# Performance work log

Hardware: AMD Instinct MI355X
Metric: run time of the kernel (lower is better)

## Reference

```python
import jax, jax.numpy as jnp
import numpy as np

B, S, D = 2, 2048, 2048
H, HD = 16, 128
P = 2048  # past (cached) kv length


def setup_inputs() -> dict:
    key = jax.random.key(0)
    ks = jax.random.split(key, 12)
    sw = 1.0 / np.sqrt(D)
    inp = {
        "x": jax.random.normal(ks[0], (B, S, D), jnp.float32),
        "past_k": jax.random.normal(ks[1], (B, H, P, HD), jnp.float32),
        "past_v": jax.random.normal(ks[2], (B, H, P, HD), jnp.float32),
        "Wq": jax.random.normal(ks[3], (D, D), jnp.float32) * sw,
        "bq": jax.random.normal(ks[4], (D,), jnp.float32) * 0.01,
        "Wk": jax.random.normal(ks[5], (D, D), jnp.float32) * sw,
        "bk": jax.random.normal(ks[6], (D,), jnp.float32) * 0.01,
        "Wv": jax.random.normal(ks[7], (D, D), jnp.float32) * sw,
        "bv": jax.random.normal(ks[8], (D,), jnp.float32) * 0.01,
        "Wo": jax.random.normal(ks[9], (D, D), jnp.float32) * sw,
        "bo": jax.random.normal(ks[10], (D,), jnp.float32) * 0.01,
    }
    return inp


def _heads(t):
    # [B, S, D] -> [B, H, S, HD]
    return t.reshape(B, -1, H, HD).transpose(0, 2, 1, 3)


def reference(x, past_k, past_v, Wq, bq, Wk, bk, Wv, bv, Wo, bo):
    # QKV projections (separate weights, _qkv_same_embed_dim=False path)
    q = _heads(x @ Wq.T + bq)          # [B,H,S,HD]
    k_new = _heads(x @ Wk.T + bk)      # [B,H,S,HD]
    v_new = _heads(x @ Wv.T + bv)

    # KV cache append
    k_cached = jnp.concatenate([past_k, k_new], axis=2)  # [B,H,P+S,HD]
    v_cached = jnp.concatenate([past_v, v_new], axis=2)
    cached_len = P + S

    # Manual attention path (query_seq_len != cached_seq_len)
    scale = 1.0 / np.sqrt(HD)
    scores = jnp.einsum('bhqd,bhkd->bhqk', q, k_cached) * scale  # [B,H,S,P+S]
    q_pos = jnp.arange(cached_len - S, cached_len)[:, None]
    k_pos = jnp.arange(cached_len)[None, :]
    mask = q_pos >= k_pos  # offset causal mask [S, P+S]
    scores = jnp.where(mask, scores, -jnp.inf)
    attn = jax.nn.softmax(scores, axis=-1)
    out = jnp.einsum('bhqk,bhkd->bhqd', attn, v_cached)  # [B,H,S,HD]

    out = out.transpose(0, 2, 1, 3).reshape(B, S, D)
    return out @ Wo.T + bo
```

## Files before the change

kernel.cpp:

```cpp
#include <hip/hip_runtime.h>

typedef unsigned short u16;
typedef __attribute__((ext_vector_type(4))) float f32x4;
typedef __attribute__((ext_vector_type(16))) float f32x16;
typedef __attribute__((ext_vector_type(8))) short s16x8;
typedef __attribute__((ext_vector_type(2))) unsigned int u32x2v;

#define CEXP 0.12751742929f

static __device__ __forceinline__ u16 f2bf(float x) {
  unsigned u = __float_as_uint(x);
  u = u + 0x7fffu + ((u >> 16) & 1u);
  return (u16)(u >> 16);
}
static __device__ __forceinline__ unsigned cvtpk(float a, float b) {
  unsigned r;
  asm("v_cvt_pk_bf16_f32 %0, %1, %2" : "=v"(r) : "v"(a), "v"(b));
  return r;
}
static __device__ __forceinline__ u32x2v pswap(unsigned a, unsigned b) {
  return __builtin_amdgcn_permlane32_swap(a, b, false, false);
}
static __device__ __forceinline__ f32x4 fzero() { f32x4 z; z[0]=0.f; z[1]=0.f; z[2]=0.f; z[3]=0.f; return z; }
static __device__ __forceinline__ f32x4 mfma16(s16x8 a, s16x8 b, f32x4 c) {
  return __builtin_amdgcn_mfma_f32_16x16x32_bf16(a, b, c, 0, 0, 0);
}
static __device__ __forceinline__ f32x16 mfma32(s16x8 a, s16x8 b, f32x16 c) {
  return __builtin_amdgcn_mfma_f32_32x32x16_bf16(a, b, c, 0, 0, 0);
}
static __device__ __forceinline__ void gld16(const void* g, void* l) {
  __builtin_amdgcn_global_load_lds((const __attribute__((address_space(1))) void*)g,
                                   (__attribute__((address_space(3))) void*)l, 16, 0, 0);
}

__global__ void cvt_kernel(const float* __restrict__ s, u16* __restrict__ d, int n4, int lg) {
  int stride = gridDim.x * blockDim.x;
  for (int i4 = blockIdx.x * blockDim.x + threadIdx.x; i4 < n4; i4 += stride) {
    int i = i4 * 4;
    float4 v = *reinterpret_cast<const float4*>(s + i);
    size_t di = (size_t)i + ((size_t)(i >> lg) << lg);
    ushort4 o;
    o.x = f2bf(v.x); o.y = f2bf(v.y); o.z = f2bf(v.z); o.w = f2bf(v.w);
    *reinterpret_cast<ushort4*>(d + di) = o;
  }
}

__global__ void transpose_past_v(const float* __restrict__ src, u16* __restrict__ dst) {
  __shared__ u16 tile[64 * 138];
  int bh = blockIdx.y, pt = blockIdx.x;
  const float* s = src + ((size_t)bh * 2048 + (size_t)pt * 64) * 128;
  int t = threadIdx.x;
#pragma unroll
  for (int it = 0; it < 8; ++it) {
    int idx = it * 1024 + t * 4;
    int row = idx >> 7, col = idx & 127;
    float4 v = *reinterpret_cast<const float4*>(s + idx);
    u16* d = &tile[row * 138 + col];
    d[0] = f2bf(v.x); d[1] = f2bf(v.y); d[2] = f2bf(v.z); d[3] = f2bf(v.w);
  }
  __syncthreads();
  size_t dbase = (size_t)bh * 128 * 4096 + (size_t)pt * 64;
#pragma unroll
  for (int it = 0; it < 32; ++it) {
    int o = it * 256 + t;
    int dd = o >> 6, pos = o & 63;
    dst[dbase + (size_t)dd * 4096 + pos] = tile[pos * 138 + dd];
  }
}

__global__ void transpose_new_v(const u16* __restrict__ src, u16* __restrict__ dst) {
  __shared__ u16 tile[64 * 138];
  int bh = blockIdx.y, pt = blockIdx.x;
  const u16* s = src + ((size_t)bh * 2048 + (size_t)pt * 64) * 128;
  int t = threadIdx.x;
#pragma unroll
  for (int it = 0; it < 8; ++it) {
    int idx = it * 1024 + t * 4;
    int row = idx >> 7, col = idx & 127;
    ushort4 v = *reinterpret_cast<const ushort4*>(s + idx);
    u16* d = &tile[row * 138 + col];
    d[0] = v.x; d[1] = v.y; d[2] = v.z; d[3] = v.w;
  }
  __syncthreads();
  size_t dbase = (size_t)bh * 128 * 4096 + 2048 + (size_t)pt * 64;
#pragma unroll
  for (int it = 0; it < 32; ++it) {
    int o = it * 256 + t;
    int dd = o >> 6, pos = o & 63;
    dst[dbase + (size_t)dd * 4096 + pos] = tile[pos * 138 + dd];
  }
}

static __device__ __forceinline__ void gemm_core(const u16* __restrict__ A, const u16* __restrict__ Wn,
                                                 int m0, char* ldsb, f32x4 (&acc)[4][4]) {
  const int tid = threadIdx.x;
  const int w = tid >> 6, lane = tid & 63, g = lane >> 4, ln = lane & 15;
#pragma unroll
  for (int mi = 0; mi < 4; ++mi)
#pragma unroll
    for (int ni = 0; ni < 4; ++ni) acc[mi][ni] = fzero();

  auto stage = [&](int buf, int k0) {
#pragma unroll
    for (int i = 0; i < 2; ++i) {
      int c = w * 2 + i;
      int p = c * 1024 + lane * 16;
      int row = p >> 6;
      int colb = (p & 63) ^ ((row & 3) << 4);
      const u16* sa = A + (size_t)(m0 + row) * 2048 + k0 + (colb >> 1);
      const u16* sw = Wn + (size_t)row * 2048 + k0 + (colb >> 1);
      char* da = ldsb + buf * 16384 + c * 1024;
      gld16(sa, da);
      gld16(sw, da + 8192);
    }
  };
  stage(0, 0);
  const int wr = w >> 1, wc = w & 1;
  for (int kt = 0; kt < 64; ++kt) {
    int cur = kt & 1;
    if (kt < 63) {
      stage(cur ^ 1, (kt + 1) * 32);
      asm volatile("s_waitcnt vmcnt(4)\n\ts_barrier" ::: "memory");
    } else {
      asm volatile("s_waitcnt vmcnt(0)\n\ts_barrier" ::: "memory");
    }
    const char* bp = ldsb + cur * 16384;
    s16x8 af[4], bw[4];
#pragma unroll
    for (int mi = 0; mi < 4; ++mi) {
      int row = wr * 64 + mi * 16 + ln;
      int lin = row * 64 + g * 16;
      af[mi] = *reinterpret_cast<const s16x8*>(bp + (lin ^ ((row & 3) << 4)));
    }
#pragma unroll
    for (int ni = 0; ni < 4; ++ni) {
      int row = wc * 64 + ni * 16 + ln;
      int lin = row * 64 + g * 16;
      bw[ni] = *reinterpret_cast<const s16x8*>(bp + 8192 + (lin ^ ((row & 3) << 4)));
    }
#pragma unroll
    for (int mi = 0; mi < 4; ++mi)
#pragma unroll
      for (int ni = 0; ni < 4; ++ni)
        acc[mi][ni] = mfma16(af[mi], bw[ni], acc[mi][ni]);
    asm volatile("s_waitcnt lgkmcnt(0)\n\ts_barrier" ::: "memory");
  }
}

__global__ __launch_bounds__(256, 3) void qkv_gemm(const u16* __restrict__ xb,
    const u16* __restrict__ wq, const u16* __restrict__ wk, const u16* __restrict__ wv,
    const float* __restrict__ bq, const float* __restrict__ bk, const float* __restrict__ bv,
    u16* __restrict__ outq, u16* __restrict__ kc, u16* __restrict__ outv) {
  __shared__ char ldsb[32768];
  int m0 = blockIdx.x * 128;
  int ny = blockIdx.y;
  int wsel = ny >> 4, n0 = (ny & 15) * 128;
  const u16* W; const float* bias; u16* dst; int lrow, off;
  if (wsel == 0)      { W = wq; bias = bq; dst = outq; lrow = 2048; off = 0; }
  else if (wsel == 1) { W = wk; bias = bk; dst = kc;   lrow = 4096; off = 2048; }
  else                { W = wv; bias = bv; dst = outv; lrow = 2048; off = 0; }
  f32x4 acc[4][4];
  gemm_core(xb, W + (size_t)n0 * 2048, m0, ldsb, acc);
  const int tid = threadIdx.x, w = tid >> 6, lane = tid & 63, g = lane >> 4, ln = lane & 15;
  const int wr = w >> 1, wc = w & 1;
#pragma unroll
  for (int ni = 0; ni < 4; ++ni) {
    int j = n0 + wc * 64 + ni * 16 + ln;
    float bcol = bias[j];
    int h = j >> 7, hd = j & 127;
#pragma unroll
    for (int mi = 0; mi < 4; ++mi) {
#pragma unroll
      for (int r = 0; r < 4; ++r) {
        int rowg = m0 + wr * 64 + mi * 16 + g * 4 + r;
        int b = rowg >> 11, s = rowg & 2047;
        float val = acc[mi][ni][r] + bcol;
        dst[((size_t)(b * 16 + h) * lrow + off + s) * 128 + hd] = f2bf(val);
      }
    }
  }
}

__global__ __launch_bounds__(256, 3) void proj_gemm(const u16* __restrict__ ao, const u16* __restrict__ wo,
    const float* __restrict__ bo, float* __restrict__ out) {
  __shared__ char ldsb[32768];
  int m0 = blockIdx.x * 128, n0 = blockIdx.y * 128;
  f32x4 acc[4][4];
  gemm_core(ao, wo + (size_t)n0 * 2048, m0, ldsb, acc);
  const int tid = threadIdx.x, w = tid >> 6, lane = tid & 63, g = lane >> 4, ln = lane & 15;
  const int wr = w >> 1, wc = w & 1;
#pragma unroll
  for (int ni = 0; ni < 4; ++ni) {
    int j = n0 + wc * 64 + ni * 16 + ln;
    float bcol = bo[j];
#pragma unroll
    for (int mi = 0; mi < 4; ++mi) {
#pragma unroll
      for (int r = 0; r < 4; ++r) {
        int rowg = m0 + wr * 64 + mi * 16 + g * 4 + r;
        out[(size_t)rowg * 2048 + j] = acc[mi][ni][r] + bcol;
      }
    }
  }
}

__global__ __launch_bounds__(256, 2) void attn_kernel(const u16* __restrict__ Qb,
    const u16* __restrict__ Kc, const u16* __restrict__ Vt, u16* __restrict__ Ao) {
  __shared__ char lds[65536];
  const int tid = threadIdx.x, w = tid >> 6, lane = tid & 63;
  const int hi = lane >> 5, l5 = lane & 31;
  const int bh = blockIdx.x;
  const int qy = blockIdx.y;
  const int qbk = (qy & 8) ? (15 - (qy & 7)) : qy;
  const int b = bh >> 4, h = bh & 15;
  const u16* Qbh = Qb + (size_t)bh * 2048 * 128;
  const u16* Kbh = Kc + (size_t)bh * 4096 * 128;
  const u16* Vbh = Vt + (size_t)bh * 128 * 4096;

  const int qrow0 = qbk * 128 + w * 32;
  const int qp = 2048 + qrow0 + l5;
  const int qpmin = 2048 + qrow0;
  const int ntiles = (2048 + qbk * 128 + 128) >> 6;

  s16x8 qf[8];
#pragma unroll
  for (int kc = 0; kc < 8; ++kc)
    qf[kc] = *reinterpret_cast<const s16x8*>(Qbh + (size_t)(qrow0 + l5) * 128 + kc * 16 + hi * 8);

  f32x16 o[4];
#pragma unroll
  for (int dt = 0; dt < 4; ++dt)
#pragma unroll
    for (int i = 0; i < 16; ++i) o[dt][i] = 0.f;
  float mrun = -3e38f, lrun = 0.f;

  auto stage = [&](int buf, int kv0) {
    char* base = lds + buf * 32768;
#pragma unroll
    for (int i = 0; i < 4; ++i) {
      int p = (w * 4 + i) * 1024 + lane * 16;
      int row = p >> 8;
      int colb = (p & 255) ^ ((row & 7) << 4);
      gld16(Kbh + (size_t)(kv0 + row) * 128 + (colb >> 1), base + (w * 4 + i) * 1024);
      int vrow = p >> 7;
      int vcol = (p & 127) ^ ((vrow & 7) << 4);
      gld16(Vbh + (size_t)vrow * 4096 + kv0 + (vcol >> 1), base + 16384 + (w * 4 + i) * 1024);
    }
  };

  stage(0, 0);
  for (int t = 0; t < ntiles; ++t) {
    const int kv0 = t * 64;
    const int cur = t & 1;
    if (t + 1 < ntiles) {
      stage(cur ^ 1, kv0 + 64);
      asm volatile("s_waitcnt vmcnt(8)\n\ts_barrier" ::: "memory");
    } else {
      asm volatile("s_waitcnt vmcnt(0)\n\ts_barrier" ::: "memory");
    }
    const char* Kl = lds + cur * 32768;
    const char* Vl = Kl + 16384;
    if (kv0 <= qpmin + 31) {
      f32x16 s0, s1;
#pragma unroll
      for (int i = 0; i < 16; ++i) { s0[i] = 0.f; s1[i] = 0.f; }
      __builtin_amdgcn_s_setprio(1);
#pragma unroll
      for (int kc = 0; kc < 8; ++kc) {
        {
          int row = l5;
          int lin = row * 256 + kc * 32 + hi * 16;
          s16x8 a = *reinterpret_cast<const s16x8*>(Kl + (lin ^ ((row & 7) << 4)));
          s0 = mfma32(a, qf[kc], s0);
        }
        {
          int row = 32 + l5;
          int lin = row * 256 + kc * 32 + hi * 16;
          s16x8 a = *reinterpret_cast<const s16x8*>(Kl + (lin ^ ((row & 7) << 4)));
          s1 = mfma32(a, qf[kc], s1);
        }
      }
      __builtin_amdgcn_s_setprio(0);
      if (kv0 + 63 > qpmin) {
#pragma unroll
        for (int i = 0; i < 16; ++i) {
          int r0 = (i & 3) + 8 * (i >> 2) + 4 * hi;
          if (kv0 + r0 > qp) s0[i] = -3e38f;
          if (kv0 + 32 + r0 > qp) s1[i] = -3e38f;
        }
      }
      float pm = fmaxf(s0[0], s0[1]);
#pragma unroll
      for (int i = 2; i < 16; i += 2) pm = fmaxf(fmaxf(pm, s0[i]), s0[i + 1]);
#pragma unroll
      for (int i = 0; i < 16; i += 2) pm = fmaxf(fmaxf(pm, s1[i]), s1[i + 1]);
      {
        u32x2v rr = pswap(__float_as_uint(pm), __float_as_uint(pm));
        pm = fmaxf(pm, __uint_as_float(hi ? rr[0] : rr[1]));
      }
      float mnew = (pm > mrun + 8.f) ? pm : mrun;
      float fsc = exp2f((mrun - mnew) * CEXP);
      mrun = mnew;
      float r0 = 0.f, r1 = 0.f, r2 = 0.f, r3 = 0.f;
#pragma unroll
      for (int i = 0; i < 16; i += 4) {
        float p0 = exp2f((s0[i] - mnew) * CEXP);
        float p1 = exp2f((s0[i + 1] - mnew) * CEXP);
        float p2 = exp2f((s0[i + 2] - mnew) * CEXP);
        float p3 = exp2f((s0[i + 3] - mnew) * CEXP);
        s0[i] = p0; s0[i + 1] = p1; s0[i + 2] = p2; s0[i + 3] = p3;
        r0 += p0; r1 += p1; r2 += p2; r3 += p3;
      }
#pragma unroll
      for (int i = 0; i < 16; i += 4) {
        float p0 = exp2f((s1[i] - mnew) * CEXP);
        float p1 = exp2f((s1[i + 1] - mnew) * CEXP);
        float p2 = exp2f((s1[i + 2] - mnew) * CEXP);
        float p3 = exp2f((s1[i + 3] - mnew) * CEXP);
        s1[i] = p0; s1[i + 1] = p1; s1[i + 2] = p2; s1[i + 3] = p3;
        r0 += p0; r1 += p1; r2 += p2; r3 += p3;
      }
      float rs = (r0 + r1) + (r2 + r3);
      {
        u32x2v rr = pswap(__float_as_uint(rs), __float_as_uint(rs));
        rs += __uint_as_float(hi ? rr[0] : rr[1]);
      }
      lrun = lrun * fsc + rs;
      if (!__all(fsc == 1.f)) {
#pragma unroll
        for (int dt = 0; dt < 4; ++dt)
#pragma unroll
          for (int i = 0; i < 16; ++i) o[dt][i] *= fsc;
      }
      s16x8 pb[4];
#pragma unroll
      for (int c2 = 0; c2 < 4; ++c2) {
        const f32x16& sv = (c2 & 2) ? s1 : s0;
        const int b0 = (c2 & 1) * 8;
        unsigned x0 = cvtpk(sv[b0 + 0], sv[b0 + 1]);
        unsigned x1 = cvtpk(sv[b0 + 2], sv[b0 + 3]);
        unsigned y0 = cvtpk(sv[b0 + 4], sv[b0 + 5]);
        unsigned y1 = cvtpk(sv[b0 + 6], sv[b0 + 7]);
        u32x2v q0 = pswap(x0, y0);
        u32x2v q1 = pswap(x1, y1);
        union { unsigned u[4]; s16x8 v; } pu;
        pu.u[0] = q0[0]; pu.u[1] = q1[0]; pu.u[2] = q0[1]; pu.u[3] = q1[1];
        pb[c2] = pu.v;
      }
      __builtin_amdgcn_s_setprio(1);
#pragma unroll
      for (int dt = 0; dt < 4; ++dt) {
#pragma unroll
        for (int c2 = 0; c2 < 4; ++c2) {
          int row = dt * 32 + l5;
          int lin = row * 128 + c2 * 32 + hi * 16;
          s16x8 va = *reinterpret_cast<const s16x8*>(Vl + (lin ^ ((row & 7) << 4)));
          o[dt] = mfma32(va, pb[c2], o[dt]);
        }
      }
      __builtin_amdgcn_s_setprio(0);
    }
    asm volatile("s_waitcnt lgkmcnt(0)\n\ts_barrier" ::: "memory");
  }

  float li = 1.f / lrun;
#pragma unroll
  for (int dt = 0; dt < 4; ++dt)
#pragma unroll
    for (int i = 0; i < 16; ++i) o[dt][i] *= li;
  const int qb = w * 32 + l5;
#pragma unroll
  for (int dt = 0; dt < 4; ++dt) {
#pragma unroll
    for (int rg = 0; rg < 4; ++rg) {
      int d0 = dt * 32 + rg * 8 + hi * 4;
      unsigned w0 = cvtpk(o[dt][rg * 4 + 0], o[dt][rg * 4 + 1]);
      unsigned w1 = cvtpk(o[dt][rg * 4 + 2], o[dt][rg * 4 + 3]);
      int lin = qb * 256 + d0 * 2;
      int phys = lin ^ ((qb & 7) << 4);
      *reinterpret_cast<uint2*>(lds + phys) = make_uint2(w0, w1);
    }
  }
  __syncthreads();
  const int qr = tid >> 4, c16 = tid & 15;
#pragma unroll
  for (int it = 0; it < 8; ++it) {
    int q = qr + it * 16;
    int phys = (q * 256 + c16 * 16) ^ ((q & 7) << 4);
    s16x8 v = *reinterpret_cast<const s16x8*>(lds + phys);
    *reinterpret_cast<s16x8*>(Ao + ((size_t)(b * 2048 + qbk * 128 + q)) * 2048 + h * 128 + c16 * 8) = v;
  }
}

extern "C" void kernel_launch(void* const* d_in, const int* in_sizes, int n_in,
                              void* d_out, int out_size, void* d_ws, size_t ws_size,
                              hipStream_t stream) {
  const float* x      = (const float*)d_in[0];
  const float* past_k = (const float*)d_in[1];
  const float* past_v = (const float*)d_in[2];
  const float* Wq = (const float*)d_in[3];
  const float* bq = (const float*)d_in[4];
  const float* Wk = (const float*)d_in[5];
  const float* bk = (const float*)d_in[6];
  const float* Wv = (const float*)d_in[7];
  const float* bv = (const float*)d_in[8];
  const float* Wo = (const float*)d_in[9];
  const float* bo = (const float*)d_in[10];
  float* out = (float*)d_out;

  char* ws = (char*)d_ws;
  u16* xb   = (u16*)(ws);
  u16* wqb  = (u16*)(ws + 16777216);
  u16* wkb  = (u16*)(ws + 25165824);
  u16* wvb  = (u16*)(ws + 33554432);
  u16* wob  = (u16*)(ws + 41943040);
  u16* kc   = (u16*)(ws + 50331648);
  u16* qbuf = (u16*)(ws + 83886080);
  u16* vn   = (u16*)(ws + 100663296);
  u16* vt   = (u16*)(ws + 117440512);
  u16* ao   = xb;

  cvt_kernel<<<1024, 256, 0, stream>>>(x, xb, 2097152, 30);
  cvt_kernel<<<1024, 256, 0, stream>>>(Wq, wqb, 1048576, 30);
  cvt_kernel<<<1024, 256, 0, stream>>>(Wk, wkb, 1048576, 30);
  cvt_kernel<<<1024, 256, 0, stream>>>(Wv, wvb, 1048576, 30);
  cvt_kernel<<<1024, 256, 0, stream>>>(Wo, wob, 1048576, 30);
  cvt_kernel<<<1024, 256, 0, stream>>>(past_k, kc, 2097152, 18);
  transpose_past_v<<<dim3(32, 32), 256, 0, stream>>>(past_v, vt);
  qkv_gemm<<<dim3(32, 48), 256, 0, stream>>>(xb, wqb, wkb, wvb, bq, bk, bv, qbuf, kc, vn);
  transpose_new_v<<<dim3(32, 32), 256, 0, stream>>>(vn, vt);
  attn_kernel<<<dim3(32, 16), 256, 0, stream>>>(qbuf, kc, vt, ao);
  proj_gemm<<<dim3(32, 16), 256, 0, stream>>>(ao, wob, bo, out);
}
```

Measured before the change: 385.0 us.

## Merge conversion launches and compute softmax row sums via MFMA with ones

The six separate fp32-to-bf16 conversion launches become one grid-stride kernel that picks source and destination by index range, which removes launch overhead and tail gaps between small kernels. In the attention kernel, the VALU row-sum reduction and cross-lane swap for the softmax denominator are dropped. The sum is instead accumulated by an extra MFMA per chunk that multiplies a ones vector by the bf16 probabilities, so the denominator now uses the same bf16-rounded values as the numerator. This trades VALU adds and a permute for four additional matrix ops per tile and an extra 16-register accumulator, which may raise register pressure.

```diff
diff --git a/kernel.cpp b/kernel.cpp
--- a/kernel.cpp
+++ b/kernel.cpp
@@ -33,12 +33,21 @@
                                    (__attribute__((address_space(3))) void*)l, 16, 0, 0);
 }
 
-__global__ void cvt_kernel(const float* __restrict__ s, u16* __restrict__ d, int n4, int lg) {
+__global__ void cvt_all(const float* __restrict__ x, const float* __restrict__ wq,
+                        const float* __restrict__ wk, const float* __restrict__ wv,
+                        const float* __restrict__ wo, const float* __restrict__ pk,
+                        u16* __restrict__ xb, u16* __restrict__ wqb, u16* __restrict__ wkb,
+                        u16* __restrict__ wvb, u16* __restrict__ wob, u16* __restrict__ kc) {
   int stride = gridDim.x * blockDim.x;
-  for (int i4 = blockIdx.x * blockDim.x + threadIdx.x; i4 < n4; i4 += stride) {
-    int i = i4 * 4;
+  for (int i4 = blockIdx.x * blockDim.x + threadIdx.x; i4 < 8388608; i4 += stride) {
+    const float* s; u16* d; int i; size_t di;
+    if (i4 < 2097152)      { i = i4 * 4;             s = x;  d = xb;  di = i; }
+    else if (i4 < 3145728) { i = (i4 - 2097152) * 4; s = wq; d = wqb; di = i; }
+    else if (i4 < 4194304) { i = (i4 - 3145728) * 4; s = wk; d = wkb; di = i; }
+    else if (i4 < 5242880) { i = (i4 - 4194304) * 4; s = wv; d = wvb; di = i; }
+    else if (i4 < 6291456) { i = (i4 - 5242880) * 4; s = wo; d = wob; di = i; }
+    else { i = (i4 - 6291456) * 4; s = pk; d = kc; di = (size_t)i + ((size_t)(i >> 18) << 18); }
     float4 v = *reinterpret_cast<const float4*>(s + i);
-    size_t di = (size_t)i + ((size_t)(i >> lg) << lg);
     ushort4 o;
     o.x = f2bf(v.x); o.y = f2bf(v.y); o.z = f2bf(v.z); o.w = f2bf(v.w);
     *reinterpret_cast<ushort4*>(d + di) = o;
@@ -227,12 +236,18 @@
   for (int kc = 0; kc < 8; ++kc)
     qf[kc] = *reinterpret_cast<const s16x8*>(Qbh + (size_t)(qrow0 + l5) * 128 + kc * 16 + hi * 8);
 
-  f32x16 o[4];
+  s16x8 ones;
+#pragma unroll
+  for (int j = 0; j < 8; ++j) ones[j] = (short)0x3F80;
+
+  f32x16 o[4], o_l;
 #pragma unroll
   for (int dt = 0; dt < 4; ++dt)
 #pragma unroll
     for (int i = 0; i < 16; ++i) o[dt][i] = 0.f;
-  float mrun = -3e38f, lrun = 0.f;
+#pragma unroll
+  for (int i = 0; i < 16; ++i) o_l[i] = 0.f;
+  float mrun = -3e38f;
 
   auto stage = [&](int buf, int kv0) {
     char* base = lds + buf * 32768;
@@ -301,36 +316,16 @@
       float mnew = (pm > mrun + 8.f) ? pm : mrun;
       float fsc = exp2f((mrun - mnew) * CEXP);
       mrun = mnew;
-      float r0 = 0.f, r1 = 0.f, r2 = 0.f, r3 = 0.f;
-#pragma unroll
-      for (int i = 0; i < 16; i += 4) {
-        float p0 = exp2f((s0[i] - mnew) * CEXP);
-        float p1 = exp2f((s0[i + 1] - mnew) * CEXP);
-        float p2 = exp2f((s0[i + 2] - mnew) * CEXP);
-        float p3 = exp2f((s0[i + 3] - mnew) * CEXP);
-        s0[i] = p0; s0[i + 1] = p1; s0[i + 2] = p2; s0[i + 3] = p3;
-        r0 += p0; r1 += p1; r2 += p2; r3 += p3;
-      }
-#pragma unroll
-      for (int i = 0; i < 16; i += 4) {
-        float p0 = exp2f((s1[i] - mnew) * CEXP);
-        float p1 = exp2f((s1[i + 1] - mnew) * CEXP);
-        float p2 = exp2f((s1[i + 2] - mnew) * CEXP);
-        float p3 = exp2f((s1[i + 3] - mnew) * CEXP);
-        s1[i] = p0; s1[i + 1] = p1; s1[i + 2] = p2; s1[i + 3] = p3;
-        r0 += p0; r1 += p1; r2 += p2; r3 += p3;
-      }
-      float rs = (r0 + r1) + (r2 + r3);
-      {
-        u32x2v rr = pswap(__float_as_uint(rs), __float_as_uint(rs));
-        rs += __uint_as_float(hi ? rr[0] : rr[1]);
-      }
-      lrun = lrun * fsc + rs;
+#pragma unroll
+      for (int i = 0; i < 16; ++i) s0[i] = exp2f((s0[i] - mnew) * CEXP);
+#pragma unroll
+      for (int i = 0; i < 16; ++i) s1[i] = exp2f((s1[i] - mnew) * CEXP);
       if (!__all(fsc == 1.f)) {
 #pragma unroll
         for (int dt = 0; dt < 4; ++dt)
 #pragma unroll
           for (int i = 0; i < 16; ++i) o[dt][i] *= fsc;
+        o_l[0] *= fsc;
       }
       s16x8 pb[4];
 #pragma unroll
@@ -358,12 +353,14 @@
           o[dt] = mfma32(va, pb[c2], o[dt]);
         }
       }
+#pragma unroll
+      for (int c2 = 0; c2 < 4; ++c2) o_l = mfma32(ones, pb[c2], o_l);
       __builtin_amdgcn_s_setprio(0);
     }
     asm volatile("s_waitcnt lgkmcnt(0)\n\ts_barrier" ::: "memory");
   }
 
-  float li = 1.f / lrun;
+  float li = 1.f / o_l[0];
 #pragma unroll
   for (int dt = 0; dt < 4; ++dt)
 #pragma unroll
@@ -420,12 +417,7 @@
   u16* vt   = (u16*)(ws + 117440512);
   u16* ao   = xb;
 
-  cvt_kernel<<<1024, 256, 0, stream>>>(x, xb, 2097152, 30);
-  cvt_kernel<<<1024, 256, 0, stream>>>(Wq, wqb, 1048576, 30);
-  cvt_kernel<<<1024, 256, 0, stream>>>(Wk, wkb, 1048576, 30);
-  cvt_kernel<<<1024, 256, 0, stream>>>(Wv, wvb, 1048576, 30);
-  cvt_kernel<<<1024, 256, 0, stream>>>(Wo, wob, 1048576, 30);
-  cvt_kernel<<<1024, 256, 0, stream>>>(past_k, kc, 2097152, 18);
+  cvt_all<<<2048, 256, 0, stream>>>(x, Wq, Wk, Wv, Wo, past_k, xb, wqb, wkb, wvb, wob, kc);
   transpose_past_v<<<dim3(32, 32), 256, 0, stream>>>(past_v, vt);
   qkv_gemm<<<dim3(32, 48), 256, 0, stream>>>(xb, wqb, wkb, wvb, bq, bk, bv, qbuf, kc, vn);
   transpose_new_v<<<dim3(32, 32), 256, 0, stream>>>(vn, vt);
```

After: 377.3 us. 2.0% less time.

## Fuse conversion launches and retile QKV GEMM to 128x256 with double buffering

Applied to the files above, without the earlier changes.

Merges the six fp32-to-bf16 conversion launches into a single grid-stride kernel, removing per-launch overhead and tail effects. Replaces the 128x128 QKV GEMM with a 512-thread 128x256 tile kernel that double-buffers 64-wide K slices in 96KB of LDS, loading each sub-tile in a contiguous layout ready for MFMA. A swizzled block index groups blocks that share N tiles. The larger tile and single block per CU trade occupancy for more operand reuse and overlap of loads with compute.

```diff
diff --git a/kernel.cpp b/kernel.cpp
--- a/kernel.cpp
+++ b/kernel.cpp
@@ -33,12 +33,21 @@
                                    (__attribute__((address_space(3))) void*)l, 16, 0, 0);
 }
 
-__global__ void cvt_kernel(const float* __restrict__ s, u16* __restrict__ d, int n4, int lg) {
+__global__ void cvt_all(const float* __restrict__ x, const float* __restrict__ wq,
+                        const float* __restrict__ wk, const float* __restrict__ wv,
+                        const float* __restrict__ wo, const float* __restrict__ pk,
+                        u16* __restrict__ xb, u16* __restrict__ wqb, u16* __restrict__ wkb,
+                        u16* __restrict__ wvb, u16* __restrict__ wob, u16* __restrict__ kc) {
   int stride = gridDim.x * blockDim.x;
-  for (int i4 = blockIdx.x * blockDim.x + threadIdx.x; i4 < n4; i4 += stride) {
-    int i = i4 * 4;
+  for (int i4 = blockIdx.x * blockDim.x + threadIdx.x; i4 < 8388608; i4 += stride) {
+    const float* s; u16* d; int i; size_t di;
+    if (i4 < 2097152)      { i = i4 * 4;             s = x;  d = xb;  di = i; }
+    else if (i4 < 3145728) { i = (i4 - 2097152) * 4; s = wq; d = wqb; di = i; }
+    else if (i4 < 4194304) { i = (i4 - 3145728) * 4; s = wk; d = wkb; di = i; }
+    else if (i4 < 5242880) { i = (i4 - 4194304) * 4; s = wv; d = wvb; di = i; }
+    else if (i4 < 6291456) { i = (i4 - 5242880) * 4; s = wo; d = wob; di = i; }
+    else { i = (i4 - 6291456) * 4; s = pk; d = kc; di = (size_t)i + ((size_t)(i >> 18) << 18); }
     float4 v = *reinterpret_cast<const float4*>(s + i);
-    size_t di = (size_t)i + ((size_t)(i >> lg) << lg);
     ushort4 o;
     o.x = f2bf(v.x); o.y = f2bf(v.y); o.z = f2bf(v.z); o.w = f2bf(v.w);
     *reinterpret_cast<ushort4*>(d + di) = o;
@@ -147,27 +156,87 @@
   }
 }
 
-__global__ __launch_bounds__(256, 3) void qkv_gemm(const u16* __restrict__ xb,
+__global__ __launch_bounds__(512, 1) void qkv_gemm8(const u16* __restrict__ xb,
     const u16* __restrict__ wq, const u16* __restrict__ wk, const u16* __restrict__ wv,
     const float* __restrict__ bq, const float* __restrict__ bk, const float* __restrict__ bv,
     u16* __restrict__ outq, u16* __restrict__ kc, u16* __restrict__ outv) {
-  __shared__ char ldsb[32768];
-  int m0 = blockIdx.x * 128;
-  int ny = blockIdx.y;
-  int wsel = ny >> 4, n0 = (ny & 15) * 128;
+  __shared__ char lds[98304];
+  const int tid = threadIdx.x;
+  const int w = tid >> 6, lane = tid & 63, g = lane >> 4, ln = lane & 15;
+  const int wr = w >> 2, wc = w & 3;
+  const int bid = blockIdx.x;
+  const int swz = (bid & 7) * 96 + (bid >> 3);
+  const int mx = swz & 31, nb = swz >> 5;
+  const int m0 = mx * 128;
+  const int wsel = nb >> 3;
+  const int n0w = (nb & 7) * 256;
   const u16* W; const float* bias; u16* dst; int lrow, off;
   if (wsel == 0)      { W = wq; bias = bq; dst = outq; lrow = 2048; off = 0; }
   else if (wsel == 1) { W = wk; bias = bk; dst = kc;   lrow = 4096; off = 2048; }
   else                { W = wv; bias = bv; dst = outv; lrow = 2048; off = 0; }
+
   f32x4 acc[4][4];
-  gemm_core(xb, W + (size_t)n0 * 2048, m0, ldsb, acc);
-  const int tid = threadIdx.x, w = tid >> 6, lane = tid & 63, g = lane >> 4, ln = lane & 15;
-  const int wr = w >> 1, wc = w & 1;
+#pragma unroll
+  for (int mi = 0; mi < 4; ++mi)
+#pragma unroll
+    for (int ni = 0; ni < 4; ++ni) acc[mi][ni] = fzero();
+
+  auto issue6 = [&](int bufoff, int kt) {
+    int k0 = kt * 64;
+#pragma unroll
+    for (int s = 0; s < 6; ++s) {
+      int c = w * 6 + s;
+      if (c < 16) {
+        int mi_g = c >> 1, ks = c & 1;
+        gld16(xb + (size_t)(m0 + mi_g * 16 + ln) * 2048 + k0 + ks * 32 + g * 8,
+              lds + bufoff + c * 1024);
+      } else {
+        int cb = c - 16;
+        int ni_g = cb >> 1, ks = cb & 1;
+        gld16(W + (size_t)(n0w + ni_g * 16 + ln) * 2048 + k0 + ks * 32 + g * 8,
+              lds + bufoff + 16384 + cb * 1024);
+      }
+    }
+  };
+  auto half = [&](int bufoff) {
+#pragma unroll
+    for (int q = 0; q < 4; ++q) {
+      int mh = q >> 1, nh = q & 1;
+      s16x8 af[2][2], bw2[2][2];
+#pragma unroll
+      for (int i = 0; i < 2; ++i)
+#pragma unroll
+        for (int ks = 0; ks < 2; ++ks) {
+          af[i][ks]  = *reinterpret_cast<const s16x8*>(
+              lds + bufoff + (((wr * 4 + mh * 2 + i) << 1) + ks) * 1024 + lane * 16);
+          bw2[i][ks] = *reinterpret_cast<const s16x8*>(
+              lds + bufoff + 16384 + (((wc * 4 + nh * 2 + i) << 1) + ks) * 1024 + lane * 16);
+        }
+#pragma unroll
+      for (int i = 0; i < 2; ++i)
+#pragma unroll
+        for (int j = 0; j < 2; ++j) {
+          acc[mh * 2 + i][nh * 2 + j] = mfma16(af[i][0], bw2[j][0], acc[mh * 2 + i][nh * 2 + j]);
+          acc[mh * 2 + i][nh * 2 + j] = mfma16(af[i][1], bw2[j][1], acc[mh * 2 + i][nh * 2 + j]);
+        }
+    }
+  };
+
+  issue6(0, 0);
+  for (int t = 0; t < 16; ++t) {
+    asm volatile("s_waitcnt vmcnt(0)\n\ts_barrier" ::: "memory");
+    issue6(49152, 2 * t + 1);
+    half(0);
+    asm volatile("s_waitcnt vmcnt(0)\n\ts_barrier" ::: "memory");
+    if (t < 15) issue6(0, 2 * t + 2);
+    half(49152);
+  }
+
 #pragma unroll
   for (int ni = 0; ni < 4; ++ni) {
-    int j = n0 + wc * 64 + ni * 16 + ln;
-    float bcol = bias[j];
-    int h = j >> 7, hd = j & 127;
+    int ncol = n0w + wc * 64 + ni * 16 + ln;
+    float bcol = bias[ncol];
+    int h = ncol >> 7, hd = ncol & 127;
 #pragma unroll
     for (int mi = 0; mi < 4; ++mi) {
 #pragma unroll
@@ -420,14 +489,9 @@
   u16* vt   = (u16*)(ws + 117440512);
   u16* ao   = xb;
 
-  cvt_kernel<<<1024, 256, 0, stream>>>(x, xb, 2097152, 30);
-  cvt_kernel<<<1024, 256, 0, stream>>>(Wq, wqb, 1048576, 30);
-  cvt_kernel<<<1024, 256, 0, stream>>>(Wk, wkb, 1048576, 30);
-  cvt_kernel<<<1024, 256, 0, stream>>>(Wv, wvb, 1048576, 30);
-  cvt_kernel<<<1024, 256, 0, stream>>>(Wo, wob, 1048576, 30);
-  cvt_kernel<<<1024, 256, 0, stream>>>(past_k, kc, 2097152, 18);
+  cvt_all<<<2048, 256, 0, stream>>>(x, Wq, Wk, Wv, Wo, past_k, xb, wqb, wkb, wvb, wob, kc);
   transpose_past_v<<<dim3(32, 32), 256, 0, stream>>>(past_v, vt);
-  qkv_gemm<<<dim3(32, 48), 256, 0, stream>>>(xb, wqb, wkb, wvb, bq, bk, bv, qbuf, kc, vn);
+  qkv_gemm8<<<768, 512, 0, stream>>>(xb, wqb, wkb, wvb, bq, bk, bv, qbuf, kc, vn);
   transpose_new_v<<<dim3(32, 32), 256, 0, stream>>>(vn, vt);
   attn_kernel<<<dim3(32, 16), 256, 0, stream>>>(qbuf, kc, vt, ao);
   proj_gemm<<<dim3(32, 16), 256, 0, stream>>>(ao, wob, bo, out);
```

New measurement: 426.4 us. +10.7%, slower.
